# Performance work log

Hardware: AMD Instinct MI355X
Metric: run time of the kernel (lower is better)

The kernel has to match this reference:

```python
import jax, jax.numpy as jnp
import numpy as np

MARGIN = 100.0

def _cdist(a, b):
    # Euclidean pairwise distances, same math as torch.cdist(p=2).
    d2 = (jnp.sum(a * a, axis=1)[:, None]
          + jnp.sum(b * b, axis=1)[None, :]
          - 2.0 * (a @ b.T))
    return jnp.sqrt(jnp.maximum(d2, 0.0))

def setup_inputs() -> dict:
    key = jax.random.key(0)
    feats = jax.random.normal(key, (16384, 256), dtype=jnp.float32)
    return {"feats": feats}

def reference(feats):
    bs = feats.shape[0]
    normal = feats[: bs // 2]      # [N, D]
    abnormal = feats[bs // 2:]     # [N, D]
    dist_n = _cdist(normal, normal)    # [N, N]
    dist_a = _cdist(normal, abnormal)  # [N, N]
    max_d_n = jnp.max(dist_n, axis=0)  # [N]
    min_d_a = jnp.min(dist_a, axis=0)  # [N]
    return jnp.mean(max_d_n) + jnp.mean(jnp.maximum(MARGIN - min_d_a, 0.0))
```

## Files before the change

### kernel.cpp

```cpp
#include <hip/hip_runtime.h>
#include <hip/hip_bf16.h>

#define NROWS 16384
#define NHALF 8192
#define KDIM  256
#define TMARGIN 100.0f

#define BM 128
#define NROWBLK (NHALF / BM)
#define NCOLSPLIT 16
#define COLS_PER_SPLIT (NROWS / NCOLSPLIT)
#define CC_ITERS (COLS_PER_SPLIT / 128)

typedef __bf16 bf16x8 __attribute__((ext_vector_type(8)));
typedef __bf16 bf16x4 __attribute__((ext_vector_type(4)));
typedef float  f32x4  __attribute__((ext_vector_type(4)));

__device__ __bf16 g_bf[NROWS * KDIM];
__device__ float  g_sq[NROWS];
__device__ float  g_part[2 * NROWBLK * NROWS];
__device__ float  g_colres[NROWS];

__global__ __launch_bounds__(256) void prep_kernel(const float* __restrict__ feats) {
    int w    = threadIdx.x >> 6;
    int lane = threadIdx.x & 63;
    int row  = blockIdx.x * 4 + w;

    const float* rp = feats + (size_t)row * KDIM + lane * 4;
    float4 v = *(const float4*)rp;

    bf16x4 b;
    b[0] = (__bf16)v.x; b[1] = (__bf16)v.y; b[2] = (__bf16)v.z; b[3] = (__bf16)v.w;
    *(bf16x4*)(g_bf + (size_t)row * KDIM + lane * 4) = b;

    float sq = v.x*v.x + v.y*v.y + v.z*v.z + v.w*v.w;
    #pragma unroll
    for (int off = 32; off > 0; off >>= 1) sq += __shfl_xor(sq, off);
    if (lane == 0) g_sq[row] = sq;
}

__global__ __launch_bounds__(256, 2) void dist_kernel() {
    __shared__ __align__(16) char smem[BM * KDIM * 2];

    int tid  = threadIdx.x;
    int w    = tid >> 6;
    int lane = tid & 63;
    int wr   = w >> 1;
    int wc   = w & 1;
    int l15  = lane & 15;
    int lh   = lane >> 4;

    int bid      = blockIdx.x;
    int colsplit = bid & (NCOLSPLIT - 1);
    int rowblk   = bid >> 4;
    bool minmode = colsplit >= (NCOLSPLIT / 2);

    {
        const __bf16* src = g_bf + (size_t)rowblk * BM * KDIM;
        #pragma unroll
        for (int i = 0; i < 16; ++i) {
            int chunk = tid + i * 256;
            int row = chunk >> 5;
            int kc  = chunk & 31;
            bf16x8 v = *(const bf16x8*)(src + row * KDIM + kc * 8);
            int dst = row * 512 + ((kc * 16) ^ ((row & 7) << 4));
            *(bf16x8*)(smem + dst) = v;
        }
    }
    __syncthreads();

    int abase[4][2];
    #pragma unroll
    for (int m = 0; m < 4; ++m) {
        int row = wr * 64 + m * 16 + l15;
        #pragma unroll
        for (int p = 0; p < 2; ++p)
            abase[m][p] = row * 512 + (((p * 64) + lh * 16) ^ ((row & 7) << 4));
    }

    float init = minmode ? 3.0e38f : -3.0e38f;
    int rowglob = rowblk * BM + wr * 64;

    for (int cc = 0; cc < CC_ITERS; ++cc) {
        int colbase = colsplit * COLS_PER_SPLIT + cc * 128 + wc * 64;

        f32x4 acc[4][4];
        #pragma unroll
        for (int m = 0; m < 4; ++m)
            #pragma unroll
            for (int n = 0; n < 4; ++n)
                acc[m][n] = (f32x4){0.f, 0.f, 0.f, 0.f};

        bf16x8 A_[2][4], B_[2][4];
        #pragma unroll
        for (int m = 0; m < 4; ++m)
            A_[0][m] = *(const bf16x8*)(smem + abase[m][0]);
        #pragma unroll
        for (int n = 0; n < 4; ++n)
            B_[0][n] = *(const bf16x8*)(g_bf + (size_t)(colbase + n * 16 + l15) * KDIM + lh * 8);

        #pragma unroll
        for (int s = 0; s < 8; ++s) {
            const int cur = s & 1, nxt = cur ^ 1;
            if (s < 7) {
                const int sp = s + 1;
                #pragma unroll
                for (int m = 0; m < 4; ++m)
                    A_[nxt][m] = *(const bf16x8*)(smem + abase[m][sp & 1] + (sp >> 1) * 128);
                #pragma unroll
                for (int n = 0; n < 4; ++n)
                    B_[nxt][n] = *(const bf16x8*)(g_bf + (size_t)(colbase + n * 16 + l15) * KDIM
                                                  + sp * 32 + lh * 8);
            }
            #pragma unroll
            for (int m = 0; m < 4; ++m)
                #pragma unroll
                for (int n = 0; n < 4; ++n)
                    acc[m][n] = __builtin_amdgcn_mfma_f32_16x16x32_bf16(
                        A_[cur][m], B_[cur][n], acc[m][n], 0, 0, 0);
        }

        float m_run[4] = {init, init, init, init};
        #pragma unroll
        for (int m = 0; m < 4; ++m) {
            f32x4 sq = *(const f32x4*)(g_sq + rowglob + m * 16 + lh * 4);
            #pragma unroll
            for (int n = 0; n < 4; ++n) {
                #pragma unroll
                for (int r = 0; r < 4; ++r) {
                    float t = sq[r] - 2.0f * acc[m][n][r];
                    m_run[n] = minmode ? fminf(m_run[n], t) : fmaxf(m_run[n], t);
                }
            }
        }
        #pragma unroll
        for (int n = 0; n < 4; ++n) {
            float v = m_run[n];
            float v1 = __shfl_xor(v, 16);
            v = minmode ? fminf(v, v1) : fmaxf(v, v1);
            v1 = __shfl_xor(v, 32);
            v = minmode ? fminf(v, v1) : fmaxf(v, v1);
            m_run[n] = v;
        }
        if (lane < 16) {
            int pslot = rowblk * 2 + wr;
            #pragma unroll
            for (int n = 0; n < 4; ++n)
                g_part[(size_t)pslot * NROWS + colbase + n * 16 + lane] = m_run[n];
        }
    }
}

__global__ __launch_bounds__(256) void finish1_kernel() {
    int col = blockIdx.x * 256 + threadIdx.x;
    bool mn = col >= NHALF;
    float m = mn ? 3.0e38f : -3.0e38f;
    for (int p = 0; p < 2 * NROWBLK; ++p) {
        float v = g_part[(size_t)p * NROWS + col];
        m = mn ? fminf(m, v) : fmaxf(m, v);
    }
    float d = sqrtf(fmaxf(m + g_sq[col], 0.f));
    g_colres[col] = mn ? fmaxf(TMARGIN - d, 0.f) : d;
}

__global__ __launch_bounds__(256) void finish2_kernel(float* __restrict__ out) {
    int tid = threadIdx.x;
    float s1 = 0.f, s2 = 0.f;
    for (int j = tid; j < NROWS; j += 256) {
        float v = g_colres[j];
        if (j < NHALF) s1 += v; else s2 += v;
    }
    #pragma unroll
    for (int off = 32; off > 0; off >>= 1) {
        s1 += __shfl_xor(s1, off);
        s2 += __shfl_xor(s2, off);
    }
    __shared__ float r1[4], r2[4];
    int w = tid >> 6, lane = tid & 63;
    if (lane == 0) { r1[w] = s1; r2[w] = s2; }
    __syncthreads();
    if (tid == 0) {
        float a = r1[0] + r1[1] + r1[2] + r1[3];
        float b = r2[0] + r2[1] + r2[2] + r2[3];
        out[0] = a / (float)NHALF + b / (float)NHALF;
    }
}

extern "C" void kernel_launch(void* const* d_in, const int* in_sizes, int n_in,
                              void* d_out, int out_size, void* d_ws, size_t ws_size,
                              hipStream_t stream) {
    const float* feats = (const float*)d_in[0];
    float* out = (float*)d_out;
    hipLaunchKernelGGL(prep_kernel,    dim3(NROWS / 4),           dim3(256), 0, stream, feats);
    hipLaunchKernelGGL(dist_kernel,    dim3(NROWBLK * NCOLSPLIT), dim3(256), 0, stream);
    hipLaunchKernelGGL(finish1_kernel, dim3(NROWS / 256),         dim3(256), 0, stream);
    hipLaunchKernelGGL(finish2_kernel, dim3(1),                   dim3(256), 0, stream, out);
}
```

Baseline: 222.3 us.

## Switch distance GEMM to 32x32x16 MFMA with per-wave full-row tiles and cross-tile prefetch

The dist kernel now has each wave cover all 128 rows of the block against its own 32 columns, using 32x32x16 bf16 MFMAs in place of 16x16x32. B fragments are prefetched across column-tile iterations, row norms are hoisted into registers once, and the cross-wave row split is removed, which halves the partial buffer and the finish1 reduction. The column split drops from 16 to 8, so there are half as many blocks, each doing more work. The aim is fewer shuffles and partial writes and better MFMA density, at the cost of higher register pressure (sqv holds 64 floats per thread) and less parallelism across the grid.

```diff
diff --git a/kernel.cpp b/kernel.cpp
--- a/kernel.cpp
+++ b/kernel.cpp
@@ -8,17 +8,17 @@
 
 #define BM 128
 #define NROWBLK (NHALF / BM)
-#define NCOLSPLIT 16
+#define NCOLSPLIT 8
 #define COLS_PER_SPLIT (NROWS / NCOLSPLIT)
 #define CC_ITERS (COLS_PER_SPLIT / 128)
 
 typedef __bf16 bf16x8 __attribute__((ext_vector_type(8)));
 typedef __bf16 bf16x4 __attribute__((ext_vector_type(4)));
-typedef float  f32x4  __attribute__((ext_vector_type(4)));
+typedef float  f32x16 __attribute__((ext_vector_type(16)));
 
 __device__ __bf16 g_bf[NROWS * KDIM];
 __device__ float  g_sq[NROWS];
-__device__ float  g_part[2 * NROWBLK * NROWS];
+__device__ float  g_part[NROWBLK * NROWS];
 __device__ float  g_colres[NROWS];
 
 __global__ __launch_bounds__(256) void prep_kernel(const float* __restrict__ feats) {
@@ -45,14 +45,12 @@
     int tid  = threadIdx.x;
     int w    = tid >> 6;
     int lane = tid & 63;
-    int wr   = w >> 1;
-    int wc   = w & 1;
-    int l15  = lane & 15;
-    int lh   = lane >> 4;
+    int l31  = lane & 31;
+    int hh   = lane >> 5;
 
     int bid      = blockIdx.x;
     int colsplit = bid & (NCOLSPLIT - 1);
-    int rowblk   = bid >> 4;
+    int rowblk   = bid >> 3;
     bool minmode = colsplit >= (NCOLSPLIT / 2);
 
     {
@@ -69,93 +67,85 @@
     }
     __syncthreads();
 
-    int abase[4][2];
+    int xorf   = (lane & 7) << 4;
+    int base_l = l31 * 512;
+    int q      = xorf & 0x60;
+    int p      = (hh * 16) ^ (xorf & 0x10);
+
+    int rowglob = rowblk * BM;
+    float sqv[4][16];
     #pragma unroll
-    for (int m = 0; m < 4; ++m) {
-        int row = wr * 64 + m * 16 + l15;
+    for (int mp = 0; mp < 4; ++mp)
         #pragma unroll
-        for (int p = 0; p < 2; ++p)
-            abase[m][p] = row * 512 + (((p * 64) + lh * 16) ^ ((row & 7) << 4));
-    }
+        for (int r = 0; r < 16; ++r)
+            sqv[mp][r] = g_sq[rowglob + mp * 32 + 4 * hh + (r & 3) + 8 * (r >> 2)];
+
+    const __bf16* bpanel = g_bf
+        + (size_t)(colsplit * COLS_PER_SPLIT + w * 32 + l31) * KDIM + hh * 8;
 
     float init = minmode ? 3.0e38f : -3.0e38f;
-    int rowglob = rowblk * BM + wr * 64;
+
+    bf16x8 A_[2][4], B_[4];
+
+#define LOADA(SLOT, S)                                                         \
+    {                                                                          \
+        int a_ = base_l + (((S) * 32) ^ q) + p;                                \
+        A_[SLOT][0] = *(const bf16x8*)(smem + a_);                             \
+        A_[SLOT][1] = *(const bf16x8*)(smem + a_ + 16384);                     \
+        A_[SLOT][2] = *(const bf16x8*)(smem + a_ + 32768);                     \
+        A_[SLOT][3] = *(const bf16x8*)(smem + a_ + 49152);                     \
+    }
+#define LOADB(SLOT, CC, S)                                                     \
+    B_[SLOT] = *(const bf16x8*)(bpanel + (size_t)(CC) * (128 * KDIM) + (S) * 16);
+
+    LOADA(0, 0);
+    LOADB(0, 0, 0); LOADB(1, 0, 1); LOADB(2, 0, 2); LOADB(3, 0, 3);
 
     for (int cc = 0; cc < CC_ITERS; ++cc) {
-        int colbase = colsplit * COLS_PER_SPLIT + cc * 128 + wc * 64;
+        int ccn = (cc + 1 < CC_ITERS) ? cc + 1 : cc;
 
-        f32x4 acc[4][4];
+        f32x16 acc[4];
         #pragma unroll
-        for (int m = 0; m < 4; ++m)
+        for (int mp = 0; mp < 4; ++mp)
             #pragma unroll
-            for (int n = 0; n < 4; ++n)
-                acc[m][n] = (f32x4){0.f, 0.f, 0.f, 0.f};
-
-        bf16x8 A_[2][4], B_[2][4];
-        #pragma unroll
-        for (int m = 0; m < 4; ++m)
-            A_[0][m] = *(const bf16x8*)(smem + abase[m][0]);
-        #pragma unroll
-        for (int n = 0; n < 4; ++n)
-            B_[0][n] = *(const bf16x8*)(g_bf + (size_t)(colbase + n * 16 + l15) * KDIM + lh * 8);
+            for (int j = 0; j < 16; ++j) acc[mp][j] = 0.f;
 
         #pragma unroll
-        for (int s = 0; s < 8; ++s) {
-            const int cur = s & 1, nxt = cur ^ 1;
-            if (s < 7) {
-                const int sp = s + 1;
-                #pragma unroll
-                for (int m = 0; m < 4; ++m)
-                    A_[nxt][m] = *(const bf16x8*)(smem + abase[m][sp & 1] + (sp >> 1) * 128);
-                #pragma unroll
-                for (int n = 0; n < 4; ++n)
-                    B_[nxt][n] = *(const bf16x8*)(g_bf + (size_t)(colbase + n * 16 + l15) * KDIM
-                                                  + sp * 32 + lh * 8);
-            }
+        for (int s = 0; s < 16; ++s) {
+            LOADA((s + 1) & 1, (s + 1) & 15);
             #pragma unroll
-            for (int m = 0; m < 4; ++m)
-                #pragma unroll
-                for (int n = 0; n < 4; ++n)
-                    acc[m][n] = __builtin_amdgcn_mfma_f32_16x16x32_bf16(
-                        A_[cur][m], B_[cur][n], acc[m][n], 0, 0, 0);
+            for (int mp = 0; mp < 4; ++mp)
+                acc[mp] = __builtin_amdgcn_mfma_f32_32x32x16_bf16(
+                    A_[s & 1][mp], B_[s & 3], acc[mp], 0, 0, 0);
+            if (s < 12) { LOADB(s & 3, cc,  s + 4);  }
+            else        { LOADB(s & 3, ccn, s - 12); }
         }
 
-        float m_run[4] = {init, init, init, init};
+        float m_run = init;
         #pragma unroll
-        for (int m = 0; m < 4; ++m) {
-            f32x4 sq = *(const f32x4*)(g_sq + rowglob + m * 16 + lh * 4);
+        for (int mp = 0; mp < 4; ++mp)
             #pragma unroll
-            for (int n = 0; n < 4; ++n) {
-                #pragma unroll
-                for (int r = 0; r < 4; ++r) {
-                    float t = sq[r] - 2.0f * acc[m][n][r];
-                    m_run[n] = minmode ? fminf(m_run[n], t) : fmaxf(m_run[n], t);
-                }
+            for (int r = 0; r < 16; ++r) {
+                float t = sqv[mp][r] - 2.0f * acc[mp][r];
+                m_run = minmode ? fminf(m_run, t) : fmaxf(m_run, t);
             }
-        }
-        #pragma unroll
-        for (int n = 0; n < 4; ++n) {
-            float v = m_run[n];
-            float v1 = __shfl_xor(v, 16);
-            v = minmode ? fminf(v, v1) : fmaxf(v, v1);
-            v1 = __shfl_xor(v, 32);
-            v = minmode ? fminf(v, v1) : fmaxf(v, v1);
-            m_run[n] = v;
-        }
-        if (lane < 16) {
-            int pslot = rowblk * 2 + wr;
-            #pragma unroll
-            for (int n = 0; n < 4; ++n)
-                g_part[(size_t)pslot * NROWS + colbase + n * 16 + lane] = m_run[n];
+        float o = __shfl_xor(m_run, 32);
+        m_run = minmode ? fminf(m_run, o) : fmaxf(m_run, o);
+
+        if (lane < 32) {
+            int colw = colsplit * COLS_PER_SPLIT + cc * 128 + w * 32;
+            g_part[(size_t)rowblk * NROWS + colw + l31] = m_run;
         }
     }
+#undef LOADA
+#undef LOADB
 }
 
 __global__ __launch_bounds__(256) void finish1_kernel() {
     int col = blockIdx.x * 256 + threadIdx.x;
     bool mn = col >= NHALF;
     float m = mn ? 3.0e38f : -3.0e38f;
-    for (int p = 0; p < 2 * NROWBLK; ++p) {
+    for (int p = 0; p < NROWBLK; ++p) {
         float v = g_part[(size_t)p * NROWS + col];
         m = mn ? fminf(m, v) : fmaxf(m, v);
     }
```

New measurement: 353.4 us. 1.59x slower.
